# Optimization experiments

Measured on AMD Instinct MI355X. Metric: run time of the kernel, lower is better.

Reference implementation:

```python
import jax, jax.numpy as jnp
import numpy as np

T, E, DIM, HID = 8192, 8, 1024, 2048


def setup_inputs() -> dict:
    key = jax.random.key(0)
    k1, k2, k3 = jax.random.split(key, 3)
    x = jax.random.normal(k1, (T, DIM), dtype=jnp.float32)
    w1 = jax.random.normal(k2, (E, HID, DIM), dtype=jnp.float32)
    w2 = jax.random.normal(k3, (E, DIM, HID), dtype=jnp.float32)
    # Tokens are pre-grouped by expert; counts must sum exactly to T.
    num_tokens_per_expert = jnp.full((E,), T // E, dtype=jnp.int32)
    return {"x": x, "w1": w1, "w2": w2, "num_tokens_per_expert": num_tokens_per_expert}


def reference(x, w1, w2, num_tokens_per_expert):
    # Faithful to torch._grouped_mm path: bf16 casts, two ragged grouped GEMMs,
    # result cast back to x.dtype.
    gs = num_tokens_per_expert.astype(jnp.int32)
    xb = x.astype(jnp.bfloat16)                                  # [T, dim]
    w1t = jnp.swapaxes(w1.astype(jnp.bfloat16), -2, -1)          # [E, dim, hid]
    w2t = jnp.swapaxes(w2.astype(jnp.bfloat16), -2, -1)          # [E, hid, dim]
    h = jax.lax.ragged_dot(xb, w1t, gs)                          # [T, hid] bf16
    out = jax.lax.ragged_dot(h, w2t, gs)                         # [T, dim] bf16
    return out.astype(x.dtype)
```

## Files before the change

### kernel.cpp

```cpp
#include <hip/hip_runtime.h>
#include <stdint.h>

#define T_TOK 8192
#define NEXP  8
#define DIMSZ 1024
#define HIDSZ 2048
#define MAX_MT (T_TOK / 128 + NEXP - 1)

typedef __attribute__((ext_vector_type(4))) float f32x4;
typedef __attribute__((ext_vector_type(8))) short s16x8;


__device__ __forceinline__ uint16_t f2bf(float f) {
  uint32_t u = __builtin_bit_cast(uint32_t, f);
  u += 0x7fffu + ((u >> 16) & 1u);
  return (uint16_t)(u >> 16);
}

__device__ __forceinline__ void gload_lds16(const uint16_t* g, const uint16_t* lds_base) {
  __builtin_amdgcn_global_load_lds(
      (const __attribute__((address_space(1))) uint32_t*)(uintptr_t)g,
      (__attribute__((address_space(3))) uint32_t*)(uint32_t)(uintptr_t)lds_base,
      16, 0, 0);
}


__global__ void cvt_all(const float* __restrict__ x, const float* __restrict__ w1,
                        const float* __restrict__ w2, uint16_t* __restrict__ xb,
                        uint16_t* __restrict__ w1b, uint16_t* __restrict__ w2b,
                        const int* __restrict__ counts, int* __restrict__ offs,
                        int* __restrict__ toffs) {
  if (blockIdx.x == 0 && threadIdx.x == 0) {
    int s = 0, ts = 0;
    for (int e = 0; e < NEXP; ++e) {
      offs[e] = s; toffs[e] = ts;
      s += counts[e]; ts += (counts[e] + 127) >> 7;
    }
    offs[NEXP] = s; toffs[NEXP] = ts;
  }
  const int b = blockIdx.x;
  const float4* src; uint2* dst; size_t base;
  if (b < 1024)      { src = (const float4*)x;  dst = (uint2*)xb;  base = (size_t)b * 2048; }
  else if (b < 3072) { src = (const float4*)w1; dst = (uint2*)w1b; base = (size_t)(b - 1024) * 2048; }
  else               { src = (const float4*)w2; dst = (uint2*)w2b; base = (size_t)(b - 3072) * 2048; }

#pragma unroll
  for (int it = 0; it < 2; ++it) {
    const size_t i0 = base + (size_t)it * 1024 + threadIdx.x;
    float4 v[4];
#pragma unroll
    for (int j = 0; j < 4; ++j) v[j] = src[i0 + j * 256];
    uint2 o[4];
#pragma unroll
    for (int j = 0; j < 4; ++j) {
      o[j].x = f2bf(v[j].x) | ((uint32_t)f2bf(v[j].y) << 16);
      o[j].y = f2bf(v[j].z) | ((uint32_t)f2bf(v[j].w) << 16);
    }
#pragma unroll
    for (int j = 0; j < 4; ++j) dst[i0 + j * 256] = o[j];
  }
}

template <bool OUT_BF16>
__global__ __launch_bounds__(256, 4)
void gemm_grouped(const uint16_t* __restrict__ A, const uint16_t* __restrict__ B,
                  void* __restrict__ C, const int* __restrict__ offs,
                  const int* __restrict__ toffs, int N, int K,
                  int mgs, int ntg, int ngx) {
  __shared__ __align__(16) uint16_t As[128 * 32];
  __shared__ __align__(16) uint16_t Bs[128 * 32];

  const int xcd  = blockIdx.x & 7;
  const int slot = blockIdx.x >> 3;
  const int mg = xcd / ngx;
  const int ng = xcd % ngx;
  const int mtg = mg * mgs + slot % mgs;
  const int nt  = ng * ntg + slot / mgs;
  if (mtg >= toffs[NEXP]) return;
  int e = 0;
#pragma unroll
  for (int i = 1; i < NEXP; ++i) e += (toffs[i] <= mtg) ? 1 : 0;
  const int mt      = mtg - toffs[e];
  const int m_start = offs[e];
  const int m_count = offs[e + 1] - m_start;
  const int m0      = mt * 128;
  int valid_m = m_count - m0;
  if (valid_m > 128) valid_m = 128;
  const int n0 = nt * 128;

  const int tid  = threadIdx.x;
  const int w    = tid >> 6;
  const int lane = tid & 63;
  const int wm = w & 1, wn = w >> 1;

  const int srow0 = w * 16 + (lane >> 2);
  const int srow1 = (w + 4) * 16 + (lane >> 2);
  const int scol  = (((lane & 3) ^ ((lane >> 3) & 3))) * 8;

  const uint16_t* gA = A + (size_t)m_start * K;
  const uint16_t* gB = B + (size_t)e * N * K;

  const int ar0 = m0 + (srow0 < valid_m ? srow0 : valid_m - 1);
  const int ar1 = m0 + (srow1 < valid_m ? srow1 : valid_m - 1);

  const uint16_t* a0p = gA + (size_t)ar0 * K + scol;
  const uint16_t* a1p = gA + (size_t)ar1 * K + scol;
  const uint16_t* b0p = gB + (size_t)(n0 + srow0) * K + scol;
  const uint16_t* b1p = gB + (size_t)(n0 + srow1) * K + scol;

  const uint16_t* lA0 = &As[w * 512];
  const uint16_t* lA1 = &As[(w + 4) * 512];
  const uint16_t* lB0 = &Bs[w * 512];
  const uint16_t* lB1 = &Bs[(w + 4) * 512];

  const int fr = lane & 15;
  const int fk = ((lane >> 4) ^ ((fr >> 1) & 3)) * 8;

  f32x4 acc[4][4];
#pragma unroll
  for (int mi = 0; mi < 4; ++mi)
#pragma unroll
    for (int ni = 0; ni < 4; ++ni) acc[mi][ni] = (f32x4){0.f, 0.f, 0.f, 0.f};

  for (int k0 = 0; k0 < K; k0 += 32) {
    __syncthreads();
    gload_lds16(a0p, lA0);
    gload_lds16(a1p, lA1);
    gload_lds16(b0p, lB0);
    gload_lds16(b1p, lB1);
    a0p += 32; a1p += 32; b0p += 32; b1p += 32;
    __syncthreads();

    s16x8 af[4], bf[4];
#pragma unroll
    for (int mi = 0; mi < 4; ++mi)
      af[mi] = *(const s16x8*)&As[(wm * 64 + mi * 16 + fr) * 32 + fk];
#pragma unroll
    for (int ni = 0; ni < 4; ++ni)
      bf[ni] = *(const s16x8*)&Bs[(wn * 64 + ni * 16 + fr) * 32 + fk];
#pragma unroll
    for (int mi = 0; mi < 4; ++mi)
#pragma unroll
      for (int ni = 0; ni < 4; ++ni)
        acc[mi][ni] = __builtin_amdgcn_mfma_f32_16x16x32_bf16(af[mi], bf[ni], acc[mi][ni], 0, 0, 0);
  }

  const int cq = (lane >> 4) * 4;
  const int cc = lane & 15;
#pragma unroll
  for (int mi = 0; mi < 4; ++mi) {
#pragma unroll
    for (int r = 0; r < 4; ++r) {
      const int rt = wm * 64 + mi * 16 + cq + r;
      if (rt < valid_m) {
        const size_t rowoff = (size_t)(m_start + m0 + rt) * N;
#pragma unroll
        for (int ni = 0; ni < 4; ++ni) {
          const int col = n0 + wn * 64 + ni * 16 + cc;
          const float v = acc[mi][ni][r];
          if (OUT_BF16) {
            ((uint16_t*)C)[rowoff + col] = f2bf(v);
          } else {
            const uint32_t b = (uint32_t)f2bf(v) << 16;
            ((float*)C)[rowoff + col] = __builtin_bit_cast(float, b);
          }
        }
      }
    }
  }
}


extern "C" void kernel_launch(void* const* d_in, const int* in_sizes, int n_in,
                              void* d_out, int out_size, void* d_ws, size_t ws_size,
                              hipStream_t stream) {
  const float* x  = (const float*)d_in[0];
  const float* w1 = (const float*)d_in[1];
  const float* w2 = (const float*)d_in[2];
  const int* cnt  = (const int*)d_in[3];
  float* out = (float*)d_out;

  char* ws = (char*)d_ws;
  uint16_t* xb  = (uint16_t*)(ws);
  uint16_t* w1b = (uint16_t*)(ws + 16777216);
  uint16_t* w2b = (uint16_t*)(ws + 50331648);
  uint16_t* h   = (uint16_t*)(ws + 83886080);
  int* offs     = (int*)(ws + 117440512);
  int* toffs    = offs + 9;

  cvt_all<<<5120, 256, 0, stream>>>(x, w1, w2, xb, w1b, w2b, cnt, offs, toffs);

  gemm_grouped<true><<<8 * 18 * 8, 256, 0, stream>>>(
      xb, w1b, (void*)h, offs, toffs, HIDSZ, DIMSZ, 18, 8, 2);

  gemm_grouped<false><<<8 * 9 * 8, 256, 0, stream>>>(
      h, w2b, (void*)out, offs, toffs, DIMSZ, HIDSZ, 9, 8, 1);
}
```

Before: 298.6 us.

## Fuse fp32-to-bf16 conversion into grouped GEMM tile loads with register prefetch

```diff
diff --git a/kernel.cpp b/kernel.cpp
--- a/kernel.cpp
+++ b/kernel.cpp
@@ -5,7 +5,6 @@
 #define NEXP  8
 #define DIMSZ 1024
 #define HIDSZ 2048
-#define MAX_MT (T_TOK / 128 + NEXP - 1)
 
 typedef __attribute__((ext_vector_type(4))) float f32x4;
 typedef __attribute__((ext_vector_type(8))) short s16x8;
@@ -17,20 +16,22 @@
   return (uint16_t)(u >> 16);
 }
 
-__device__ __forceinline__ void gload_lds16(const uint16_t* g, const uint16_t* lds_base) {
-  __builtin_amdgcn_global_load_lds(
-      (const __attribute__((address_space(1))) uint32_t*)(uintptr_t)g,
-      (__attribute__((address_space(3))) uint32_t*)(uint32_t)(uintptr_t)lds_base,
-      16, 0, 0);
-}
-
-
-__global__ void cvt_all(const float* __restrict__ x, const float* __restrict__ w1,
-                        const float* __restrict__ w2, uint16_t* __restrict__ xb,
-                        uint16_t* __restrict__ w1b, uint16_t* __restrict__ w2b,
-                        const int* __restrict__ counts, int* __restrict__ offs,
-                        int* __restrict__ toffs) {
-  if (blockIdx.x == 0 && threadIdx.x == 0) {
+#if __has_builtin(__builtin_amdgcn_cvt_pk_bf16_f32)
+typedef __attribute__((ext_vector_type(2))) __bf16 bf16x2;
+__device__ __forceinline__ uint32_t pk2(float a, float b) {
+  bf16x2 r = __builtin_amdgcn_cvt_pk_bf16_f32(a, b);
+  return __builtin_bit_cast(uint32_t, r);
+}
+#else
+__device__ __forceinline__ uint32_t pk2(float a, float b) {
+  return (uint32_t)f2bf(a) | ((uint32_t)f2bf(b) << 16);
+}
+#endif
+
+
+__global__ void offs_kernel(const int* __restrict__ counts, int* __restrict__ offs,
+                            int* __restrict__ toffs) {
+  if (threadIdx.x == 0) {
     int s = 0, ts = 0;
     for (int e = 0; e < NEXP; ++e) {
       offs[e] = s; toffs[e] = ts;
@@ -38,43 +39,21 @@
     }
     offs[NEXP] = s; toffs[NEXP] = ts;
   }
-  const int b = blockIdx.x;
-  const float4* src; uint2* dst; size_t base;
-  if (b < 1024)      { src = (const float4*)x;  dst = (uint2*)xb;  base = (size_t)b * 2048; }
-  else if (b < 3072) { src = (const float4*)w1; dst = (uint2*)w1b; base = (size_t)(b - 1024) * 2048; }
-  else               { src = (const float4*)w2; dst = (uint2*)w2b; base = (size_t)(b - 3072) * 2048; }
-
-#pragma unroll
-  for (int it = 0; it < 2; ++it) {
-    const size_t i0 = base + (size_t)it * 1024 + threadIdx.x;
-    float4 v[4];
-#pragma unroll
-    for (int j = 0; j < 4; ++j) v[j] = src[i0 + j * 256];
-    uint2 o[4];
-#pragma unroll
-    for (int j = 0; j < 4; ++j) {
-      o[j].x = f2bf(v[j].x) | ((uint32_t)f2bf(v[j].y) << 16);
-      o[j].y = f2bf(v[j].z) | ((uint32_t)f2bf(v[j].w) << 16);
-    }
-#pragma unroll
-    for (int j = 0; j < 4; ++j) dst[i0 + j * 256] = o[j];
-  }
-}
-
-template <bool OUT_BF16>
-__global__ __launch_bounds__(256, 4)
-void gemm_grouped(const uint16_t* __restrict__ A, const uint16_t* __restrict__ B,
+}
+
+template <bool A_BF16, bool OUT_BF16>
+__global__ __launch_bounds__(256, 3)
+void gemm_grouped(const void* __restrict__ Av, const float* __restrict__ Bf,
                   void* __restrict__ C, const int* __restrict__ offs,
                   const int* __restrict__ toffs, int N, int K,
-                  int mgs, int ntg, int ngx) {
+                  int mgs, int ntg, int ngx, int ngm) {
   __shared__ __align__(16) uint16_t As[128 * 32];
   __shared__ __align__(16) uint16_t Bs[128 * 32];
 
   const int xcd  = blockIdx.x & 7;
   const int slot = blockIdx.x >> 3;
-  const int mg = xcd / ngx;
-  const int ng = xcd % ngx;
-  const int mtg = mg * mgs + slot % mgs;
+  const int mg = xcd / ngx, ng = xcd % ngx;
+  const int mtg = mg + ngm * (slot % mgs);
   const int nt  = ng * ntg + slot / mgs;
   if (mtg >= toffs[NEXP]) return;
   int e = 0;
@@ -89,29 +68,66 @@
   const int n0 = nt * 128;
 
   const int tid  = threadIdx.x;
+  const int lane = tid & 63;
   const int w    = tid >> 6;
-  const int lane = tid & 63;
   const int wm = w & 1, wn = w >> 1;
 
-  const int srow0 = w * 16 + (lane >> 2);
-  const int srow1 = (w + 4) * 16 + (lane >> 2);
-  const int scol  = (((lane & 3) ^ ((lane >> 3) & 3))) * 8;
-
-  const uint16_t* gA = A + (size_t)m_start * K;
-  const uint16_t* gB = B + (size_t)e * N * K;
-
-  const int ar0 = m0 + (srow0 < valid_m ? srow0 : valid_m - 1);
-  const int ar1 = m0 + (srow1 < valid_m ? srow1 : valid_m - 1);
-
-  const uint16_t* a0p = gA + (size_t)ar0 * K + scol;
-  const uint16_t* a1p = gA + (size_t)ar1 * K + scol;
-  const uint16_t* b0p = gB + (size_t)(n0 + srow0) * K + scol;
-  const uint16_t* b1p = gB + (size_t)(n0 + srow1) * K + scol;
-
-  const uint16_t* lA0 = &As[w * 512];
-  const uint16_t* lA1 = &As[(w + 4) * 512];
-  const uint16_t* lB0 = &Bs[w * 512];
-  const uint16_t* lB1 = &Bs[(w + 4) * 512];
+  const int r0 = tid >> 2;
+  const int r1 = r0 + 64;
+  const int qc = tid & 3;
+  const int s0 = (r0 >> 1) & 3, s1 = (r1 >> 1) & 3;
+  uint16_t* wA0 = &As[r0 * 32 + (qc ^ s0) * 8];
+  uint16_t* wA1 = &As[r1 * 32 + (qc ^ s1) * 8];
+  uint16_t* wB0 = &Bs[r0 * 32 + (qc ^ s0) * 8];
+  uint16_t* wB1 = &Bs[r1 * 32 + (qc ^ s1) * 8];
+
+  const int ar0 = m_start + m0 + (r0 < valid_m ? r0 : valid_m - 1);
+  const int ar1 = m_start + m0 + (r1 < valid_m ? r1 : valid_m - 1);
+
+  const float*    aF0 = nullptr; const float*    aF1 = nullptr;
+  const uint16_t* aH0 = nullptr; const uint16_t* aH1 = nullptr;
+  if constexpr (A_BF16) {
+    aH0 = (const uint16_t*)Av + (size_t)ar0 * K + qc * 8;
+    aH1 = (const uint16_t*)Av + (size_t)ar1 * K + qc * 8;
+  } else {
+    aF0 = (const float*)Av + (size_t)ar0 * K + qc * 8;
+    aF1 = (const float*)Av + (size_t)ar1 * K + qc * 8;
+  }
+  const float* bP0 = Bf + ((size_t)e * N + n0 + r0) * K + qc * 8;
+  const float* bP1 = Bf + ((size_t)e * N + n0 + r1) * K + qc * 8;
+
+  f32x4 a_f[4]; uint4 a_h[2]; f32x4 b_f[4];
+
+  auto load_tiles = [&]() {
+    if constexpr (A_BF16) {
+      a_h[0] = *(const uint4*)aH0;
+      a_h[1] = *(const uint4*)aH1;
+      aH0 += 32; aH1 += 32;
+    } else {
+      a_f[0] = *(const f32x4*)aF0; a_f[1] = *(const f32x4*)(aF0 + 4);
+      a_f[2] = *(const f32x4*)aF1; a_f[3] = *(const f32x4*)(aF1 + 4);
+      aF0 += 32; aF1 += 32;
+    }
+    b_f[0] = *(const f32x4*)bP0; b_f[1] = *(const f32x4*)(bP0 + 4);
+    b_f[2] = *(const f32x4*)bP1; b_f[3] = *(const f32x4*)(bP1 + 4);
+    bP0 += 32; bP1 += 32;
+  };
+
+  auto store_lds = [&]() {
+    if constexpr (A_BF16) {
+      *(uint4*)wA0 = a_h[0];
+      *(uint4*)wA1 = a_h[1];
+    } else {
+      *(uint4*)wA0 = make_uint4(pk2(a_f[0][0], a_f[0][1]), pk2(a_f[0][2], a_f[0][3]),
+                                pk2(a_f[1][0], a_f[1][1]), pk2(a_f[1][2], a_f[1][3]));
+      *(uint4*)wA1 = make_uint4(pk2(a_f[2][0], a_f[2][1]), pk2(a_f[2][2], a_f[2][3]),
+                                pk2(a_f[3][0], a_f[3][1]), pk2(a_f[3][2], a_f[3][3]));
+    }
+    *(uint4*)wB0 = make_uint4(pk2(b_f[0][0], b_f[0][1]), pk2(b_f[0][2], b_f[0][3]),
+                              pk2(b_f[1][0], b_f[1][1]), pk2(b_f[1][2], b_f[1][3]));
+    *(uint4*)wB1 = make_uint4(pk2(b_f[2][0], b_f[2][1]), pk2(b_f[2][2], b_f[2][3]),
+                              pk2(b_f[3][0], b_f[3][1]), pk2(b_f[3][2], b_f[3][3]));
+  };
 
   const int fr = lane & 15;
   const int fk = ((lane >> 4) ^ ((fr >> 1) & 3)) * 8;
@@ -122,14 +138,13 @@
 #pragma unroll
     for (int ni = 0; ni < 4; ++ni) acc[mi][ni] = (f32x4){0.f, 0.f, 0.f, 0.f};
 
-  for (int k0 = 0; k0 < K; k0 += 32) {
+  load_tiles();
+  const int iters = K >> 5;
+  for (int it = 0; it < iters; ++it) {
     __syncthreads();
-    gload_lds16(a0p, lA0);
-    gload_lds16(a1p, lA1);
-    gload_lds16(b0p, lB0);
-    gload_lds16(b1p, lB1);
-    a0p += 32; a1p += 32; b0p += 32; b1p += 32;
+    store_lds();
     __syncthreads();
+    if (it + 1 < iters) load_tiles();
 
     s16x8 af[4], bf[4];
 #pragma unroll
@@ -181,18 +196,15 @@
   float* out = (float*)d_out;
 
   char* ws = (char*)d_ws;
-  uint16_t* xb  = (uint16_t*)(ws);
-  uint16_t* w1b = (uint16_t*)(ws + 16777216);
-  uint16_t* w2b = (uint16_t*)(ws + 50331648);
-  uint16_t* h   = (uint16_t*)(ws + 83886080);
-  int* offs     = (int*)(ws + 117440512);
-  int* toffs    = offs + 9;
-
-  cvt_all<<<5120, 256, 0, stream>>>(x, w1, w2, xb, w1b, w2b, cnt, offs, toffs);
-
-  gemm_grouped<true><<<8 * 18 * 8, 256, 0, stream>>>(
-      xb, w1b, (void*)h, offs, toffs, HIDSZ, DIMSZ, 18, 8, 2);
-
-  gemm_grouped<false><<<8 * 9 * 8, 256, 0, stream>>>(
-      h, w2b, (void*)out, offs, toffs, DIMSZ, HIDSZ, 9, 8, 1);
-}
+  uint16_t* h = (uint16_t*)ws;
+  int* offs   = (int*)(ws + 33554432);
+  int* toffs  = offs + 9;
+
+  offs_kernel<<<1, 64, 0, stream>>>(cnt, offs, toffs);
+
+  gemm_grouped<false, true><<<8 * 18 * 8, 256, 0, stream>>>(
+      (const void*)x, w1, (void*)h, offs, toffs, HIDSZ, DIMSZ, 18, 8, 2, 4);
+
+  gemm_grouped<true, false><<<8 * 9 * 8, 256, 0, stream>>>(
+      (const void*)h, w2, (void*)out, offs, toffs, DIMSZ, HIDSZ, 9, 8, 1, 8);
+}
```

Result: slower. 408.8 us (+36.9%).

## Double GEMM K-tile to 64 with new LDS swizzle, widen conversion stores

Applied to the files above, without the earlier changes.

```diff
diff --git a/kernel.cpp b/kernel.cpp
--- a/kernel.cpp
+++ b/kernel.cpp
@@ -5,7 +5,7 @@
 #define NEXP  8
 #define DIMSZ 1024
 #define HIDSZ 2048
-#define MAX_MT (T_TOK / 128 + NEXP - 1)
+#define BK    64
 
 typedef __attribute__((ext_vector_type(4))) float f32x4;
 typedef __attribute__((ext_vector_type(8))) short s16x8;
@@ -39,25 +39,29 @@
     offs[NEXP] = s; toffs[NEXP] = ts;
   }
   const int b = blockIdx.x;
-  const float4* src; uint2* dst; size_t base;
-  if (b < 1024)      { src = (const float4*)x;  dst = (uint2*)xb;  base = (size_t)b * 2048; }
-  else if (b < 3072) { src = (const float4*)w1; dst = (uint2*)w1b; base = (size_t)(b - 1024) * 2048; }
-  else               { src = (const float4*)w2; dst = (uint2*)w2b; base = (size_t)(b - 3072) * 2048; }
-
-#pragma unroll
-  for (int it = 0; it < 2; ++it) {
-    const size_t i0 = base + (size_t)it * 1024 + threadIdx.x;
-    float4 v[4];
-#pragma unroll
-    for (int j = 0; j < 4; ++j) v[j] = src[i0 + j * 256];
-    uint2 o[4];
+  const float4* src; uint4* dst; size_t base;
+  if (b < 512)       { src = (const float4*)x;  dst = (uint4*)xb;  base = (size_t)b * 2048; }
+  else if (b < 1536) { src = (const float4*)w1; dst = (uint4*)w1b; base = (size_t)(b - 512) * 2048; }
+  else               { src = (const float4*)w2; dst = (uint4*)w2b; base = (size_t)(b - 1536) * 2048; }
+
+#pragma unroll
+  for (int half = 0; half < 2; ++half) {
+    const size_t u0 = base + (size_t)half * 1024 + threadIdx.x;
+    float4 v[8];
 #pragma unroll
     for (int j = 0; j < 4; ++j) {
-      o[j].x = f2bf(v[j].x) | ((uint32_t)f2bf(v[j].y) << 16);
-      o[j].y = f2bf(v[j].z) | ((uint32_t)f2bf(v[j].w) << 16);
-    }
-#pragma unroll
-    for (int j = 0; j < 4; ++j) dst[i0 + j * 256] = o[j];
+      v[2 * j]     = src[2 * (u0 + j * 256)];
+      v[2 * j + 1] = src[2 * (u0 + j * 256) + 1];
+    }
+#pragma unroll
+    for (int j = 0; j < 4; ++j) {
+      uint4 o;
+      o.x = f2bf(v[2 * j].x)     | ((uint32_t)f2bf(v[2 * j].y) << 16);
+      o.y = f2bf(v[2 * j].z)     | ((uint32_t)f2bf(v[2 * j].w) << 16);
+      o.z = f2bf(v[2 * j + 1].x) | ((uint32_t)f2bf(v[2 * j + 1].y) << 16);
+      o.w = f2bf(v[2 * j + 1].z) | ((uint32_t)f2bf(v[2 * j + 1].w) << 16);
+      dst[u0 + j * 256] = o;
+    }
   }
 }
 
@@ -67,13 +71,12 @@
                   void* __restrict__ C, const int* __restrict__ offs,
                   const int* __restrict__ toffs, int N, int K,
                   int mgs, int ntg, int ngx) {
-  __shared__ __align__(16) uint16_t As[128 * 32];
-  __shared__ __align__(16) uint16_t Bs[128 * 32];
+  __shared__ __align__(16) uint16_t As[128 * BK];
+  __shared__ __align__(16) uint16_t Bs[128 * BK];
 
   const int xcd  = blockIdx.x & 7;
   const int slot = blockIdx.x >> 3;
-  const int mg = xcd / ngx;
-  const int ng = xcd % ngx;
+  const int mg = xcd / ngx, ng = xcd % ngx;
   const int mtg = mg * mgs + slot % mgs;
   const int nt  = ng * ntg + slot / mgs;
   if (mtg >= toffs[NEXP]) return;
@@ -89,32 +92,29 @@
   const int n0 = nt * 128;
 
   const int tid  = threadIdx.x;
+  const int lane = tid & 63;
   const int w    = tid >> 6;
-  const int lane = tid & 63;
   const int wm = w & 1, wn = w >> 1;
 
-  const int srow0 = w * 16 + (lane >> 2);
-  const int srow1 = (w + 4) * 16 + (lane >> 2);
-  const int scol  = (((lane & 3) ^ ((lane >> 3) & 3))) * 8;
-
+  const int srow = tid >> 3;
+  const int gch  = (tid & 7) ^ (srow & 7);
+  const uint16_t* gB = B + (size_t)e * N * K;
   const uint16_t* gA = A + (size_t)m_start * K;
-  const uint16_t* gB = B + (size_t)e * N * K;
-
-  const int ar0 = m0 + (srow0 < valid_m ? srow0 : valid_m - 1);
-  const int ar1 = m0 + (srow1 < valid_m ? srow1 : valid_m - 1);
-
-  const uint16_t* a0p = gA + (size_t)ar0 * K + scol;
-  const uint16_t* a1p = gA + (size_t)ar1 * K + scol;
-  const uint16_t* b0p = gB + (size_t)(n0 + srow0) * K + scol;
-  const uint16_t* b1p = gB + (size_t)(n0 + srow1) * K + scol;
-
-  const uint16_t* lA0 = &As[w * 512];
-  const uint16_t* lA1 = &As[(w + 4) * 512];
-  const uint16_t* lB0 = &Bs[w * 512];
-  const uint16_t* lB1 = &Bs[(w + 4) * 512];
+
+  const uint16_t* aP[4];
+  const uint16_t* bP[4];
+#pragma unroll
+  for (int q = 0; q < 4; ++q) {
+    const int rq = q * 32 + srow;
+    const int ar = m0 + (rq < valid_m ? rq : valid_m - 1);
+    aP[q] = gA + (size_t)ar * K + gch * 8;
+    bP[q] = gB + (size_t)(n0 + q * 32 + srow) * K + gch * 8;
+  }
 
   const int fr = lane & 15;
-  const int fk = ((lane >> 4) ^ ((fr >> 1) & 3)) * 8;
+  const int q4 = lane >> 4;
+  const int pA0 = ((q4)     ^ (fr & 7)) * 8;
+  const int pA1 = ((4 + q4) ^ (fr & 7)) * 8;
 
   f32x4 acc[4][4];
 #pragma unroll
@@ -122,27 +122,36 @@
 #pragma unroll
     for (int ni = 0; ni < 4; ++ni) acc[mi][ni] = (f32x4){0.f, 0.f, 0.f, 0.f};
 
-  for (int k0 = 0; k0 < K; k0 += 32) {
+  for (int k0 = 0; k0 < K; k0 += BK) {
     __syncthreads();
-    gload_lds16(a0p, lA0);
-    gload_lds16(a1p, lA1);
-    gload_lds16(b0p, lB0);
-    gload_lds16(b1p, lB1);
-    a0p += 32; a1p += 32; b0p += 32; b1p += 32;
+#pragma unroll
+    for (int q = 0; q < 4; ++q) {
+      gload_lds16(aP[q], As + q * 2048 + w * 512);
+      gload_lds16(bP[q], Bs + q * 2048 + w * 512);
+      aP[q] += BK; bP[q] += BK;
+    }
     __syncthreads();
 
-    s16x8 af[4], bf[4];
-#pragma unroll
-    for (int mi = 0; mi < 4; ++mi)
-      af[mi] = *(const s16x8*)&As[(wm * 64 + mi * 16 + fr) * 32 + fk];
-#pragma unroll
-    for (int ni = 0; ni < 4; ++ni)
-      bf[ni] = *(const s16x8*)&Bs[(wn * 64 + ni * 16 + fr) * 32 + fk];
-#pragma unroll
-    for (int mi = 0; mi < 4; ++mi)
-#pragma unroll
-      for (int ni = 0; ni < 4; ++ni)
-        acc[mi][ni] = __builtin_amdgcn_mfma_f32_16x16x32_bf16(af[mi], bf[ni], acc[mi][ni], 0, 0, 0);
+    s16x8 af[4][2], bf[4][2];
+#pragma unroll
+    for (int mi = 0; mi < 4; ++mi) {
+      const int r = (wm * 64 + mi * 16 + fr) * BK;
+      af[mi][0] = *(const s16x8*)&As[r + pA0];
+      af[mi][1] = *(const s16x8*)&As[r + pA1];
+    }
+#pragma unroll
+    for (int ni = 0; ni < 4; ++ni) {
+      const int r = (wn * 64 + ni * 16 + fr) * BK;
+      bf[ni][0] = *(const s16x8*)&Bs[r + pA0];
+      bf[ni][1] = *(const s16x8*)&Bs[r + pA1];
+    }
+#pragma unroll
+    for (int t = 0; t < 2; ++t)
+#pragma unroll
+      for (int mi = 0; mi < 4; ++mi)
+#pragma unroll
+        for (int ni = 0; ni < 4; ++ni)
+          acc[mi][ni] = __builtin_amdgcn_mfma_f32_16x16x32_bf16(af[mi][t], bf[ni][t], acc[mi][ni], 0, 0, 0);
   }
 
   const int cq = (lane >> 4) * 4;
@@ -161,8 +170,8 @@
           if (OUT_BF16) {
             ((uint16_t*)C)[rowoff + col] = f2bf(v);
           } else {
-            const uint32_t b = (uint32_t)f2bf(v) << 16;
-            ((float*)C)[rowoff + col] = __builtin_bit_cast(float, b);
+            const uint32_t bb = (uint32_t)f2bf(v) << 16;
+            ((float*)C)[rowoff + col] = __builtin_bit_cast(float, bb);
           }
         }
       }
@@ -188,7 +197,7 @@
   int* offs     = (int*)(ws + 117440512);
   int* toffs    = offs + 9;
 
-  cvt_all<<<5120, 256, 0, stream>>>(x, w1, w2, xb, w1b, w2b, cnt, offs, toffs);
+  cvt_all<<<2560, 256, 0, stream>>>(x, w1, w2, xb, w1b, w2b, cnt, offs, toffs);
 
   gemm_grouped<true><<<8 * 18 * 8, 256, 0, stream>>>(
       xb, w1b, (void*)h, offs, toffs, HIDSZ, DIMSZ, 18, 8, 2);
```

After: 290.0 us. -2.9%, faster.
